# Kernel optimization log

Measured on AMD Instinct MI355X. Metric: run time of the kernel, lower is better.

Reference implementation:

```python
import jax, jax.numpy as jnp
import numpy as np

K = 4            # max_k: top-k proposals kept per gt
IOU_THRESH = 0.6 # Matcher threshold; labels [0,1]


def box_cxcywh_to_xyxy(b):
    cx, cy, w, h = jnp.split(b, 4, axis=-1)
    return jnp.concatenate([cx - 0.5 * w, cy - 0.5 * h, cx + 0.5 * w, cy + 0.5 * h], axis=-1)


def box_iou(b1, b2):
    # b1: [M,4], b2: [N,4] xyxy -> iou [M,N]
    area1 = (b1[:, 2] - b1[:, 0]) * (b1[:, 3] - b1[:, 1])
    area2 = (b2[:, 2] - b2[:, 0]) * (b2[:, 3] - b2[:, 1])
    lt = jnp.maximum(b1[:, None, :2], b2[None, :, :2])
    rb = jnp.minimum(b1[:, None, 2:], b2[None, :, 2:])
    wh = jnp.clip(rb - lt, 0.0)
    inter = wh[..., 0] * wh[..., 1]
    union = area1[:, None] + area2[None, :] - inter
    return inter / jnp.maximum(union, 1e-9)


def setup_inputs() -> dict:
    key = jax.random.key(0)
    k1, k2, k3 = jax.random.split(key, 3)
    B, M, N = 32, 512, 4096
    gt_boxes = jax.random.uniform(k1, (B, M, 4), dtype=jnp.float32)
    proposals = jax.random.uniform(k2, (B, N, 4), dtype=jnp.float32)
    gt_labels = jax.random.randint(k3, (B, M), 0, 80, dtype=jnp.int32)
    return {"gt_boxes": gt_boxes, "proposals": proposals, "gt_labels": gt_labels}


def reference(gt_boxes, proposals, gt_labels):
    # gt_boxes: [B,M,4] cxcywh, proposals: [B,N,4] cxcywh (init_reference)
    B, M, _ = gt_boxes.shape
    N = proposals.shape[1]

    iou = jax.vmap(box_iou)(box_cxcywh_to_xyxy(gt_boxes),
                            box_cxcywh_to_xyxy(proposals))  # [B,M,N]

    # Matcher(thresholds=[0.6], labels=[0,1], allow_low_quality_matches=True)
    matched_idxs = jnp.argmax(iou, axis=1)                 # [B,N] best gt per proposal
    matched_vals = jnp.max(iou, axis=1)                    # [B,N]
    fg = matched_vals >= IOU_THRESH                        # matched_labels == 1
    # low-quality matches: proposals achieving the per-gt max IoU are forced fg
    max_per_gt = jnp.max(iou, axis=2, keepdims=True)       # [B,M,1]
    lq = jnp.any(iou == max_per_gt, axis=1)                # [B,N]
    pos_mask = fg | lq                                     # foreground proposals
    # (labels in [0,80) never equal bg_label=400, matched_labels never -1,
    #  and subsample keeps all fg since num_fg << 0.25*num_queries, so
    #  pos_pr_inds == all foreground proposals.)

    # counts[b,g] = number of fg proposals matched to gt g (unique(return_counts))
    counts = jnp.zeros((B, M), jnp.int32).at[
        jnp.arange(B)[:, None], matched_idxs].add(pos_mask.astype(jnp.int32))

    # sample_topk_per_gt: per-gt top-k by IoU, keep first min(count, k)
    scores, pr_inds = jax.lax.top_k(iou, K)                # [B,M,K]
    valid = jnp.arange(K)[None, None, :] < counts[:, :, None]  # [B,M,K]
    gt_inds = jnp.broadcast_to(jnp.arange(M)[None, :, None], (B, M, K))
    scores = jnp.where(valid, scores, 0.0)
    return scores, pr_inds, gt_inds, valid
```

## Files before the change

### kernel.cpp

```cpp
#include <hip/hip_runtime.h>

#define BB 32
#define MM 512
#define NN 4096
#define KK 4
#define MLO 0.999998f
#define CMG 0.9999995f
#define FG_BITS 0x3F19999A


__device__ __forceinline__ int rfl(int x) {
    return __builtin_amdgcn_readfirstlane(x);
}
__device__ __forceinline__ float rflf(float x) {
    return __int_as_float(rfl(__float_as_int(x)));
}

__device__ __forceinline__ bool beatsI(int v1, int i1, int v2, int i2) {
    return (v1 > v2) || (v1 == v2 && i1 < i2);
}

#define CE(av, ai, bv, bi)                                        \
    {                                                             \
        bool _s = beatsI(bv, bi, av, ai);                         \
        int _mv = _s ? bv : av, _nv = _s ? av : bv;               \
        int _mi = _s ? bi : ai, _ni = _s ? ai : bi;               \
        av = _mv; bv = _nv; ai = _mi; bi = _ni;                   \
    }

struct T4 { int v0, v1, v2, v3; int i0, i1, i2, i3; float thr, c1, thrga; };

__global__ __launch_bounds__(256) void kernA(const float* __restrict__ gt,
                                             const float* __restrict__ pr,
                                             float* __restrict__ topv,
                                             float4* __restrict__ pack,
                                             int* __restrict__ counts,
                                             float* __restrict__ out) {
    const int b = blockIdx.x >> 6;
    const int mblk = blockIdx.x & 63;
    const int tid = threadIdx.x;
    const int wave = rfl(tid >> 6), lane = tid & 63;
    const int mbase = mblk * 8 + wave * 2;
    const float4* g4 = (const float4*)(gt + (size_t)b * MM * 4);
    const float4* p4 = (const float4*)(pr + (size_t)b * NN * 4);

#define GTDEF(G) \
    float gx1_##G, gy1_##G, gx2_##G, gy2_##G, ga_##G; \
    { float4 gg = g4[mbase + G]; \
      float x1 = gg.x - 0.5f * gg.z, y1 = gg.y - 0.5f * gg.w; \
      float x2 = gg.x + 0.5f * gg.z, y2 = gg.y + 0.5f * gg.w; \
      gx1_##G = x1; gy1_##G = y1; gx2_##G = x2; gy2_##G = y2; \
      ga_##G = __fmul_rn(x2 - x1, y2 - y1); }

    GTDEF(0) GTDEF(1)

    T4 t0, t1;

#define PIOU(G, VB) \
    int VB; \
    { float ltx = fmaxf(gx1_##G, px1), lty = fmaxf(gy1_##G, py1); \
      float rbx = fminf(gx2_##G, px2), rby = fminf(gy2_##G, py2); \
      float wc = fmaxf(rbx - ltx, 0.0f), hc = fmaxf(rby - lty, 0.0f); \
      float inter = __fmul_rn(wc, hc); \
      float u = fmaxf((ga_##G + pa) - inter, 1e-9f); \
      VB = __float_as_int(inter / u); }

#define PRIME(T, VB, G) \
    { int x0 = VB, x1 = -1, x2 = -1, x3 = -1; \
      int y0 = lane, y1 = 0x7fffffff, y2 = 0x7fffffff, y3 = 0x7fffffff; \
      for (int off = 1; off < 64; off <<= 1) { \
        int b0 = __shfl_xor(x0, off), b1 = __shfl_xor(x1, off); \
        int b2 = __shfl_xor(x2, off), b3 = __shfl_xor(x3, off); \
        int j0 = __shfl_xor(y0, off), j1 = __shfl_xor(y1, off); \
        int j2 = __shfl_xor(y2, off), j3 = __shfl_xor(y3, off); \
        int z4 = b3, z5 = b2, z6 = b1, z7 = b0; \
        int w4 = j3, w5 = j2, w6 = j1, w7 = j0; \
        CE(x0, y0, z4, w4); CE(x1, y1, z5, w5); \
        CE(x2, y2, z6, w6); CE(x3, y3, z7, w7); \
        CE(x0, y0, x2, y2); CE(x1, y1, x3, y3); \
        CE(x0, y0, x1, y1); CE(x2, y2, x3, y3); \
      } \
      T.v0 = rfl(x0); T.v1 = rfl(x1); T.v2 = rfl(x2); T.v3 = rfl(x3); \
      T.i0 = rfl(y0); T.i1 = rfl(y1); T.i2 = rfl(y2); T.i3 = rfl(y3); \
      T.thr = (T.v3 <= 0) ? 0.0f : rflf(__int_as_float(T.v3) * MLO); \
      T.c1 = 1.0f + T.thr; T.thrga = T.thr * ga_##G; }

    {
        float4 qc = p4[lane];
        float px1 = qc.x - 0.5f * qc.z, py1 = qc.y - 0.5f * qc.w;
        float px2 = qc.x + 0.5f * qc.z, py2 = qc.y + 0.5f * qc.w;
        float pa = __fmul_rn(px2 - px1, py2 - py1);
        PIOU(0, vb0) PIOU(1, vb1)
        PRIME(t0, vb0, 0) PRIME(t1, vb1, 1)
    }

#define COMP(T, G, IN, TR) \
    float IN; bool TR; \
    { float ltx = fmaxf(gx1_##G, px1), lty = fmaxf(gy1_##G, py1); \
      float rbx = fminf(gx2_##G, px2), rby = fminf(gy2_##G, py2); \
      float wc = fmaxf(rbx - ltx, 0.0f), hc = fmaxf(rby - lty, 0.0f); \
      IN = __fmul_rn(wc, hc); \
      TR = IN * T.c1 > __fmaf_rn(T.thr, pa, T.thrga); }

#define MERGE(T, G, MK, IN, TR) \
    if (MK) { \
      float iouv = 0.0f; \
      if (TR) { float uu = fmaxf((ga_##G + pa) - IN, 1e-9f); iouv = IN / uu; } \
      unsigned long long mk = MK; \
      do { \
        int l = __ffsll((unsigned long long)mk) - 1; mk &= mk - 1; \
        int vb = (int)__builtin_amdgcn_readlane(__float_as_int(iouv), l); \
        if (vb > T.v3) {                           \
          int n = nb + l; \
          bool c2 = vb > T.v2, c1c = vb > T.v1, c0 = vb > T.v0; \
          T.v3 = c2 ? T.v2 : vb;                T.i3 = c2 ? T.i2 : n; \
          T.v2 = c2 ? (c1c ? T.v1 : vb) : T.v2; T.i2 = c2 ? (c1c ? T.i1 : n) : T.i2; \
          T.v1 = c1c ? (c0 ? T.v0 : vb) : T.v1; T.i1 = c1c ? (c0 ? T.i0 : n) : T.i1; \
          T.v0 = c0 ? vb : T.v0;                T.i0 = c0 ? n : T.i0; \
        } \
      } while (mk); \
      T.thr = (T.v3 == 0) ? 0.0f : rflf(__int_as_float(T.v3) * MLO); \
      T.c1 = 1.0f + T.thr; T.thrga = T.thr * ga_##G; \
    }

    float4 qn = p4[64 + lane];
    for (int j = 1; j < 64; ++j) {
        float4 qc = qn;
        int jn = (j < 63) ? j + 1 : 63;
        qn = p4[jn * 64 + lane];
        float px1 = qc.x - 0.5f * qc.z, py1 = qc.y - 0.5f * qc.w;
        float px2 = qc.x + 0.5f * qc.z, py2 = qc.y + 0.5f * qc.w;
        float pa = __fmul_rn(px2 - px1, py2 - py1);
        const int nb = j * 64;
        COMP(t0, 0, in0, tr0)
        COMP(t1, 1, in1, tr1)
        unsigned long long mk0 = __ballot(tr0), mk1 = __ballot(tr1);
        if (mk0 | mk1) {
            MERGE(t0, 0, mk0, in0, tr0)
            MERGE(t1, 1, mk1, in1, tr1)
        }
    }

    if (lane == 0) {
        float* pi = out + (size_t)BB * MM * KK;
        float* gi = out + (size_t)2 * BB * MM * KK;
#define WOUT(T, G) \
        { int gm = b * MM + mbase + G; \
          float gmxf = __int_as_float(T.v0); \
          topv[gm * KK + 0] = gmxf; \
          topv[gm * KK + 1] = __int_as_float(T.v1); \
          topv[gm * KK + 2] = __int_as_float(T.v2); \
          topv[gm * KK + 3] = __int_as_float(T.v3); \
          pi[gm * KK + 0] = (float)T.i0; pi[gm * KK + 1] = (float)T.i1; \
          pi[gm * KK + 2] = (float)T.i2; pi[gm * KK + 3] = (float)T.i3; \
          float fm = (float)(mbase + G); \
          gi[gm * KK + 0] = fm; gi[gm * KK + 1] = fm; \
          gi[gm * KK + 2] = fm; gi[gm * KK + 3] = fm; \
          pack[gm * 2 + 0] = make_float4(gx1_##G, gy1_##G, gx2_##G, gy2_##G); \
          pack[gm * 2 + 1] = make_float4(ga_##G, gmxf, gmxf * CMG, 0.0f); \
          counts[gm] = 0; }
        WOUT(t0, 0) WOUT(t1, 1)
    }
}

__global__ __launch_bounds__(256) void kernB(const float* __restrict__ pr,
                                             const float4* __restrict__ pack,
                                             int* __restrict__ counts) {
    __shared__ float4 sG[MM];
    __shared__ float4 sA[MM];
    __shared__ int sV[256], sI[256], sL[256];
    const int b = blockIdx.x >> 6;
    const int nblk = blockIdx.x & 63;
    const int tid = threadIdx.x;

    const float4* gp = pack + (size_t)b * MM * 2;
    for (int i = tid; i < MM; i += 256) {
        sG[i] = gp[i * 2];
        sA[i] = gp[i * 2 + 1];
    }

    const int lane = tid & 63;
    const int qtr = tid >> 6;
    const int m0 = qtr * 128;
    const int n = nblk * 64 + lane;
    float4 qq = ((const float4*)(pr + (size_t)b * NN * 4))[n];
    const float qx1 = qq.x - 0.5f * qq.z, qy1 = qq.y - 0.5f * qq.w;
    const float qx2 = qq.x + 0.5f * qq.z, qy2 = qq.y + 0.5f * qq.w;
    const float pa = __fmul_rn(qx2 - qx1, qy2 - qy1);
    __syncthreads();

    float INb = 0.0f, ub = 1.0f;
    int mb = m0;
    bool closeacc = false;
    int ms = m0, cnt = 0;

    #pragma unroll 4
    for (int mm = 0; mm < 128; ++mm) {
        const int m = m0 + mm;
        float4 gb = sG[m];
        float4 ax = sA[m];
        float ltx = fmaxf(gb.x, qx1), lty = fmaxf(gb.y, qy1);
        float rbx = fminf(gb.z, qx2), rby = fminf(gb.w, qy2);
        float w = fmaxf(rbx - ltx, 0.0f), h = fmaxf(rby - lty, 0.0f);
        float IN = __fmul_rn(w, h);
        float u = fmaxf((ax.x + pa) - IN, 1e-9f);
        float t1 = __fmul_rn(IN, ub);
        float t2 = __fmul_rn(INb, u);
        bool c = t1 > t2;
        closeacc = closeacc || ((t1 > t2 * CMG) && (t2 > t1 * CMG));
        INb = c ? IN : INb;
        ub = c ? u : ub;
        mb = c ? m : mb;
        bool cd = IN >= __fmul_rn(u, ax.z);
        ms = cd ? m : ms;
        cnt += cd ? 1 : 0;
    }

    float bestE;
    {
        float4 gb = sG[mb]; float4 ax = sA[mb];
        float ltx = fmaxf(gb.x, qx1), lty = fmaxf(gb.y, qy1);
        float rbx = fminf(gb.z, qx2), rby = fminf(gb.w, qy2);
        float w = fmaxf(rbx - ltx, 0.0f), h = fmaxf(rby - lty, 0.0f);
        float IN = __fmul_rn(w, h);
        float u = fmaxf((ax.x + pa) - IN, 1e-9f);
        bestE = IN / u;
    }
    bool lqF;
    {
        float4 gb = sG[ms]; float4 ax = sA[ms];
        float ltx = fmaxf(gb.x, qx1), lty = fmaxf(gb.y, qy1);
        float rbx = fminf(gb.z, qx2), rby = fminf(gb.w, qy2);
        float w = fmaxf(rbx - ltx, 0.0f), h = fmaxf(rby - lty, 0.0f);
        float IN = __fmul_rn(w, h);
        float u = fmaxf((ax.x + pa) - IN, 1e-9f);
        lqF = (cnt > 0) && ((IN / u) == ax.y);
    }
    bool need = closeacc || ((cnt >= 2) && !lqF);
    if (__ballot(need) != 0ull) {
        if (need) {
            float bb = 0.0f; int bi = m0; bool ll = false;
            for (int mm = 0; mm < 128; ++mm) {
                const int m = m0 + mm;
                float4 gb = sG[m]; float4 ax = sA[m];
                float ltx = fmaxf(gb.x, qx1), lty = fmaxf(gb.y, qy1);
                float rbx = fminf(gb.z, qx2), rby = fminf(gb.w, qy2);
                float w = fmaxf(rbx - ltx, 0.0f), h = fmaxf(rby - lty, 0.0f);
                float IN = __fmul_rn(w, h);
                float u = fmaxf((ax.x + pa) - IN, 1e-9f);
                float iou = IN / u;
                bool c = iou > bb;
                bb = c ? iou : bb;
                bi = c ? m : bi;
                ll = ll || (iou == ax.y);
            }
            bestE = bb; mb = bi; lqF = ll;
        }
    }

    sV[tid] = __float_as_int(bestE);
    sI[tid] = mb;
    sL[tid] = lqF ? 1 : 0;
    __syncthreads();

    if (tid < 64) {
        int v = sV[tid], i = sI[tid], L = sL[tid];
        #pragma unroll
        for (int q_ = 1; q_ < 4; ++q_) {
            int v2 = sV[tid + q_ * 64], i2 = sI[tid + q_ * 64];
            L |= sL[tid + q_ * 64];
            bool c = v2 > v;
            v = c ? v2 : v;
            i = c ? i2 : i;
        }
        if (v >= FG_BITS || L) {
            atomicAdd(&counts[b * MM + i], 1);
        }
    }
}

__global__ __launch_bounds__(256) void kernC(const float* __restrict__ topv,
                                             const int* __restrict__ counts,
                                             float* __restrict__ out) {
    const int gm = blockIdx.x * 256 + threadIdx.x;
    if (gm >= BB * MM) return;
    const int cnt = counts[gm];
    float* sc = out;
    float* va = out + (size_t)3 * BB * MM * KK;
    #pragma unroll
    for (int k = 0; k < KK; ++k) {
        const bool val = k < cnt;
        sc[gm * KK + k] = val ? topv[gm * KK + k] : 0.0f;
        va[gm * KK + k] = val ? 1.0f : 0.0f;
    }
}

extern "C" void kernel_launch(void* const* d_in, const int* in_sizes, int n_in,
                              void* d_out, int out_size, void* d_ws, size_t ws_size,
                              hipStream_t stream) {
    const float* gt = (const float*)d_in[0];
    const float* pr = (const float*)d_in[1];
    float* out = (float*)d_out;
    char* ws = (char*)d_ws;

    int*    counts = (int*)(ws);
    float*  topv   = (float*)(ws + (1 << 16));
    float4* pack   = (float4*)(ws + (5 << 16));

    kernA<<<BB * (MM / 8), 256, 0, stream>>>(gt, pr, topv, pack, counts, out);
    kernB<<<BB * (NN / 64), 256, 0, stream>>>(pr, pack, counts);
    kernC<<<(BB * MM + 255) / 256, 256, 0, stream>>>(topv, counts, out);
}
```

Measured before the change: 112.2 us.

## Fuse per-gt top-k and per-proposal argmax into one launch, scatter low-quality flags

Kernels A and B become a single launch with two disjoint block ranges, so the per-proposal argmax no longer waits for the per-gt top-k and the two can run concurrently. The per-proposal pass no longer needs the per-gt max, so its low-quality equality check is dropped. Instead a new kernel D scatters low-quality flags from each gt's top-k entries that tie the max, falling back to a full scan over proposals when all four tie. Kernel E then counts matches. This adds two small launches and extra workspace traffic, and the serial full-scan fallback in D could be slow when it is triggered.

```diff
diff --git a/kernel.cpp b/kernel.cpp
--- a/kernel.cpp
+++ b/kernel.cpp
@@ -7,6 +7,7 @@
 #define MLO 0.999998f
 #define CMG 0.9999995f
 #define FG_BITS 0x3F19999A
+#define NA_BLOCKS (BB * (MM / 8))
 
 
 __device__ __forceinline__ int rfl(int x) {
@@ -30,19 +31,28 @@
 
 struct T4 { int v0, v1, v2, v3; int i0, i1, i2, i3; float thr, c1, thrga; };
 
-__global__ __launch_bounds__(256) void kernA(const float* __restrict__ gt,
-                                             const float* __restrict__ pr,
-                                             float* __restrict__ topv,
-                                             float4* __restrict__ pack,
-                                             int* __restrict__ counts,
-                                             float* __restrict__ out) {
-    const int b = blockIdx.x >> 6;
-    const int mblk = blockIdx.x & 63;
-    const int tid = threadIdx.x;
-    const int wave = rfl(tid >> 6), lane = tid & 63;
-    const int mbase = mblk * 8 + wave * 2;
-    const float4* g4 = (const float4*)(gt + (size_t)b * MM * 4);
-    const float4* p4 = (const float4*)(pr + (size_t)b * NN * 4);
+__global__ __launch_bounds__(256) void kernAB(const float* __restrict__ gt,
+                                              const float* __restrict__ pr,
+                                              float* __restrict__ topv,
+                                              int* __restrict__ topi,
+                                              int* __restrict__ counts,
+                                              int* __restrict__ bestv,
+                                              int* __restrict__ bidxA,
+                                              unsigned char* __restrict__ lqflag,
+                                              int* __restrict__ allLq,
+                                              float* __restrict__ out) {
+    __shared__ float4 sG[MM];
+    __shared__ float sAr[MM];
+    __shared__ int sV[256], sI[256];
+
+    if (blockIdx.x < NA_BLOCKS) {
+        const int b = blockIdx.x >> 6;
+        const int mblk = blockIdx.x & 63;
+        const int tid = threadIdx.x;
+        const int wave = rfl(tid >> 6), lane = tid & 63;
+        const int mbase = mblk * 8 + wave * 2;
+        const float4* g4 = (const float4*)(gt + (size_t)b * MM * 4);
+        const float4* p4 = (const float4*)(pr + (size_t)b * NN * 4);
 
 #define GTDEF(G) \
     float gx1_##G, gy1_##G, gx2_##G, gy2_##G, ga_##G; \
@@ -52,9 +62,9 @@
       gx1_##G = x1; gy1_##G = y1; gx2_##G = x2; gy2_##G = y2; \
       ga_##G = __fmul_rn(x2 - x1, y2 - y1); }
 
-    GTDEF(0) GTDEF(1)
-
-    T4 t0, t1;
+        GTDEF(0) GTDEF(1)
+
+        T4 t0, t1;
 
 #define PIOU(G, VB) \
     int VB; \
@@ -85,14 +95,14 @@
       T.thr = (T.v3 <= 0) ? 0.0f : rflf(__int_as_float(T.v3) * MLO); \
       T.c1 = 1.0f + T.thr; T.thrga = T.thr * ga_##G; }
 
-    {
-        float4 qc = p4[lane];
-        float px1 = qc.x - 0.5f * qc.z, py1 = qc.y - 0.5f * qc.w;
-        float px2 = qc.x + 0.5f * qc.z, py2 = qc.y + 0.5f * qc.w;
-        float pa = __fmul_rn(px2 - px1, py2 - py1);
-        PIOU(0, vb0) PIOU(1, vb1)
-        PRIME(t0, vb0, 0) PRIME(t1, vb1, 1)
-    }
+        {
+            float4 qc = p4[lane];
+            float px1 = qc.x - 0.5f * qc.z, py1 = qc.y - 0.5f * qc.w;
+            float px2 = qc.x + 0.5f * qc.z, py2 = qc.y + 0.5f * qc.w;
+            float pa = __fmul_rn(px2 - px1, py2 - py1);
+            PIOU(0, vb0) PIOU(1, vb1)
+            PRIME(t0, vb0, 0) PRIME(t1, vb1, 1)
+        }
 
 #define COMP(T, G, IN, TR) \
     float IN; bool TR; \
@@ -110,7 +120,7 @@
       do { \
         int l = __ffsll((unsigned long long)mk) - 1; mk &= mk - 1; \
         int vb = (int)__builtin_amdgcn_readlane(__float_as_int(iouv), l); \
-        if (vb > T.v3) {                           \
+        if (vb > T.v3) { \
           int n = nb + l; \
           bool c2 = vb > T.v2, c1c = vb > T.v1, c0 = vb > T.v0; \
           T.v3 = c2 ? T.v2 : vb;                T.i3 = c2 ? T.i2 : n; \
@@ -123,160 +133,192 @@
       T.c1 = 1.0f + T.thr; T.thrga = T.thr * ga_##G; \
     }
 
-    float4 qn = p4[64 + lane];
-    for (int j = 1; j < 64; ++j) {
-        float4 qc = qn;
-        int jn = (j < 63) ? j + 1 : 63;
-        qn = p4[jn * 64 + lane];
-        float px1 = qc.x - 0.5f * qc.z, py1 = qc.y - 0.5f * qc.w;
-        float px2 = qc.x + 0.5f * qc.z, py2 = qc.y + 0.5f * qc.w;
-        float pa = __fmul_rn(px2 - px1, py2 - py1);
-        const int nb = j * 64;
-        COMP(t0, 0, in0, tr0)
-        COMP(t1, 1, in1, tr1)
-        unsigned long long mk0 = __ballot(tr0), mk1 = __ballot(tr1);
-        if (mk0 | mk1) {
-            MERGE(t0, 0, mk0, in0, tr0)
-            MERGE(t1, 1, mk1, in1, tr1)
-        }
-    }
-
-    if (lane == 0) {
-        float* pi = out + (size_t)BB * MM * KK;
-        float* gi = out + (size_t)2 * BB * MM * KK;
+        float4 qn = p4[64 + lane];
+        for (int j = 1; j < 64; ++j) {
+            float4 qc = qn;
+            int jn = (j < 63) ? j + 1 : 63;
+            qn = p4[jn * 64 + lane];
+            float px1 = qc.x - 0.5f * qc.z, py1 = qc.y - 0.5f * qc.w;
+            float px2 = qc.x + 0.5f * qc.z, py2 = qc.y + 0.5f * qc.w;
+            float pa = __fmul_rn(px2 - px1, py2 - py1);
+            const int nb = j * 64;
+            COMP(t0, 0, in0, tr0)
+            COMP(t1, 1, in1, tr1)
+            unsigned long long mk0 = __ballot(tr0), mk1 = __ballot(tr1);
+            if (mk0 | mk1) {
+                MERGE(t0, 0, mk0, in0, tr0)
+                MERGE(t1, 1, mk1, in1, tr1)
+            }
+        }
+
+        if (lane == 0) {
+            float* pi = out + (size_t)BB * MM * KK;
+            float* gi = out + (size_t)2 * BB * MM * KK;
 #define WOUT(T, G) \
-        { int gm = b * MM + mbase + G; \
-          float gmxf = __int_as_float(T.v0); \
-          topv[gm * KK + 0] = gmxf; \
-          topv[gm * KK + 1] = __int_as_float(T.v1); \
-          topv[gm * KK + 2] = __int_as_float(T.v2); \
-          topv[gm * KK + 3] = __int_as_float(T.v3); \
-          pi[gm * KK + 0] = (float)T.i0; pi[gm * KK + 1] = (float)T.i1; \
-          pi[gm * KK + 2] = (float)T.i2; pi[gm * KK + 3] = (float)T.i3; \
-          float fm = (float)(mbase + G); \
-          gi[gm * KK + 0] = fm; gi[gm * KK + 1] = fm; \
-          gi[gm * KK + 2] = fm; gi[gm * KK + 3] = fm; \
-          pack[gm * 2 + 0] = make_float4(gx1_##G, gy1_##G, gx2_##G, gy2_##G); \
-          pack[gm * 2 + 1] = make_float4(ga_##G, gmxf, gmxf * CMG, 0.0f); \
-          counts[gm] = 0; }
-        WOUT(t0, 0) WOUT(t1, 1)
-    }
-}
-
-__global__ __launch_bounds__(256) void kernB(const float* __restrict__ pr,
-                                             const float4* __restrict__ pack,
+            { int gm = b * MM + mbase + G; \
+              topv[gm * KK + 0] = __int_as_float(T.v0); \
+              topv[gm * KK + 1] = __int_as_float(T.v1); \
+              topv[gm * KK + 2] = __int_as_float(T.v2); \
+              topv[gm * KK + 3] = __int_as_float(T.v3); \
+              topi[gm * KK + 0] = T.i0; topi[gm * KK + 1] = T.i1; \
+              topi[gm * KK + 2] = T.i2; topi[gm * KK + 3] = T.i3; \
+              pi[gm * KK + 0] = (float)T.i0; pi[gm * KK + 1] = (float)T.i1; \
+              pi[gm * KK + 2] = (float)T.i2; pi[gm * KK + 3] = (float)T.i3; \
+              float fm = (float)(mbase + G); \
+              gi[gm * KK + 0] = fm; gi[gm * KK + 1] = fm; \
+              gi[gm * KK + 2] = fm; gi[gm * KK + 3] = fm; \
+              counts[gm] = 0; }
+            WOUT(t0, 0) WOUT(t1, 1)
+        }
+    } else {
+        const int bid = blockIdx.x - NA_BLOCKS;
+        const int b = bid >> 6;
+        const int nblk = bid & 63;
+        const int tid = threadIdx.x;
+        const float4* g4 = (const float4*)(gt + (size_t)b * MM * 4);
+
+        for (int i = tid; i < MM; i += 256) {
+            float4 gg = g4[i];
+            float x1 = gg.x - 0.5f * gg.z, y1 = gg.y - 0.5f * gg.w;
+            float x2 = gg.x + 0.5f * gg.z, y2 = gg.y + 0.5f * gg.w;
+            sG[i] = make_float4(x1, y1, x2, y2);
+            sAr[i] = __fmul_rn(x2 - x1, y2 - y1);
+        }
+        if (tid < 64) lqflag[(size_t)b * NN + nblk * 64 + tid] = 0;
+        if (tid == 0 && nblk == 0) allLq[b] = 0;
+
+        const int lane = tid & 63;
+        const int qtr = tid >> 6;
+        const int m0 = qtr * 128;
+        const int n = nblk * 64 + lane;
+        float4 qq = ((const float4*)(pr + (size_t)b * NN * 4))[n];
+        const float qx1 = qq.x - 0.5f * qq.z, qy1 = qq.y - 0.5f * qq.w;
+        const float qx2 = qq.x + 0.5f * qq.z, qy2 = qq.y + 0.5f * qq.w;
+        const float pa = __fmul_rn(qx2 - qx1, qy2 - qy1);
+        __syncthreads();
+
+        float INb = 0.0f, ub = 1.0f;
+        int mb = m0;
+        bool closeacc = false;
+
+        #pragma unroll 4
+        for (int mm = 0; mm < 128; ++mm) {
+            const int m = m0 + mm;
+            float4 gb = sG[m];
+            float ar = sAr[m];
+            float ltx = fmaxf(gb.x, qx1), lty = fmaxf(gb.y, qy1);
+            float rbx = fminf(gb.z, qx2), rby = fminf(gb.w, qy2);
+            float w = fmaxf(rbx - ltx, 0.0f), h = fmaxf(rby - lty, 0.0f);
+            float IN = __fmul_rn(w, h);
+            float u = fmaxf((ar + pa) - IN, 1e-9f);
+            float t1 = __fmul_rn(IN, ub);
+            float t2 = __fmul_rn(INb, u);
+            bool c = t1 > t2;
+            closeacc = closeacc || ((t1 > t2 * CMG) && (t2 > t1 * CMG));
+            INb = c ? IN : INb;
+            ub = c ? u : ub;
+            mb = c ? m : mb;
+        }
+
+        float bestE;
+        {
+            float4 gb = sG[mb];
+            float ltx = fmaxf(gb.x, qx1), lty = fmaxf(gb.y, qy1);
+            float rbx = fminf(gb.z, qx2), rby = fminf(gb.w, qy2);
+            float w = fmaxf(rbx - ltx, 0.0f), h = fmaxf(rby - lty, 0.0f);
+            float IN = __fmul_rn(w, h);
+            float u = fmaxf((sAr[mb] + pa) - IN, 1e-9f);
+            bestE = IN / u;
+        }
+        if (__ballot(closeacc) != 0ull) {
+            if (closeacc) {
+                float bb = 0.0f; int bi = m0;
+                for (int mm = 0; mm < 128; ++mm) {
+                    const int m = m0 + mm;
+                    float4 gb = sG[m];
+                    float ltx = fmaxf(gb.x, qx1), lty = fmaxf(gb.y, qy1);
+                    float rbx = fminf(gb.z, qx2), rby = fminf(gb.w, qy2);
+                    float w = fmaxf(rbx - ltx, 0.0f), h = fmaxf(rby - lty, 0.0f);
+                    float IN = __fmul_rn(w, h);
+                    float u = fmaxf((sAr[m] + pa) - IN, 1e-9f);
+                    float iou = IN / u;
+                    bool c = iou > bb;
+                    bb = c ? iou : bb;
+                    bi = c ? m : bi;
+                }
+                bestE = bb; mb = bi;
+            }
+        }
+
+        sV[tid] = __float_as_int(bestE);
+        sI[tid] = mb;
+        __syncthreads();
+
+        if (tid < 64) {
+            int v = sV[tid], i = sI[tid];
+            #pragma unroll
+            for (int q_ = 1; q_ < 4; ++q_) {
+                int v2 = sV[tid + q_ * 64], i2 = sI[tid + q_ * 64];
+                bool c = v2 > v;
+                v = c ? v2 : v;
+                i = c ? i2 : i;
+            }
+            const size_t pidx = (size_t)b * NN + nblk * 64 + tid;
+            bestv[pidx] = v;
+            bidxA[pidx] = i;
+        }
+    }
+}
+
+__global__ __launch_bounds__(256) void kernD(const float* __restrict__ topv,
+                                             const int* __restrict__ topi,
+                                             const float* __restrict__ gt,
+                                             const float* __restrict__ pr,
+                                             unsigned char* __restrict__ lqflag,
+                                             int* __restrict__ allLq) {
+    const int gm = blockIdx.x * 256 + threadIdx.x;
+    if (gm >= BB * MM) return;
+    const int b = gm >> 9, m = gm & (MM - 1);
+    const float v0 = topv[gm * KK + 0];
+    if (v0 == 0.0f) { allLq[b] = 1; return; }
+    unsigned char* fl = lqflag + (size_t)b * NN;
+    fl[topi[gm * KK + 0]] = 1;
+    const float v1 = topv[gm * KK + 1], v2 = topv[gm * KK + 2], v3 = topv[gm * KK + 3];
+    if (v1 == v0) fl[topi[gm * KK + 1]] = 1;
+    if (v2 == v0) fl[topi[gm * KK + 2]] = 1;
+    if (v3 == v0) {
+        fl[topi[gm * KK + 3]] = 1;
+        float4 gg = ((const float4*)(gt + (size_t)b * MM * 4))[m];
+        float x1 = gg.x - 0.5f * gg.z, y1 = gg.y - 0.5f * gg.w;
+        float x2 = gg.x + 0.5f * gg.z, y2 = gg.y + 0.5f * gg.w;
+        float ga = __fmul_rn(x2 - x1, y2 - y1);
+        const float4* p4 = (const float4*)(pr + (size_t)b * NN * 4);
+        for (int n = 0; n < NN; ++n) {
+            float4 qc = p4[n];
+            float px1 = qc.x - 0.5f * qc.z, py1 = qc.y - 0.5f * qc.w;
+            float px2 = qc.x + 0.5f * qc.z, py2 = qc.y + 0.5f * qc.w;
+            float pa = __fmul_rn(px2 - px1, py2 - py1);
+            float ltx = fmaxf(x1, px1), lty = fmaxf(y1, py1);
+            float rbx = fminf(x2, px2), rby = fminf(y2, py2);
+            float w = fmaxf(rbx - ltx, 0.0f), h = fmaxf(rby - lty, 0.0f);
+            float IN = __fmul_rn(w, h);
+            float u = fmaxf((ga + pa) - IN, 1e-9f);
+            if ((IN / u) == v0) fl[n] = 1;
+        }
+    }
+}
+
+__global__ __launch_bounds__(256) void kernE(const int* __restrict__ bestv,
+                                             const int* __restrict__ bidxA,
+                                             const unsigned char* __restrict__ lqflag,
+                                             const int* __restrict__ allLq,
                                              int* __restrict__ counts) {
-    __shared__ float4 sG[MM];
-    __shared__ float4 sA[MM];
-    __shared__ int sV[256], sI[256], sL[256];
-    const int b = blockIdx.x >> 6;
-    const int nblk = blockIdx.x & 63;
-    const int tid = threadIdx.x;
-
-    const float4* gp = pack + (size_t)b * MM * 2;
-    for (int i = tid; i < MM; i += 256) {
-        sG[i] = gp[i * 2];
-        sA[i] = gp[i * 2 + 1];
-    }
-
-    const int lane = tid & 63;
-    const int qtr = tid >> 6;
-    const int m0 = qtr * 128;
-    const int n = nblk * 64 + lane;
-    float4 qq = ((const float4*)(pr + (size_t)b * NN * 4))[n];
-    const float qx1 = qq.x - 0.5f * qq.z, qy1 = qq.y - 0.5f * qq.w;
-    const float qx2 = qq.x + 0.5f * qq.z, qy2 = qq.y + 0.5f * qq.w;
-    const float pa = __fmul_rn(qx2 - qx1, qy2 - qy1);
-    __syncthreads();
-
-    float INb = 0.0f, ub = 1.0f;
-    int mb = m0;
-    bool closeacc = false;
-    int ms = m0, cnt = 0;
-
-    #pragma unroll 4
-    for (int mm = 0; mm < 128; ++mm) {
-        const int m = m0 + mm;
-        float4 gb = sG[m];
-        float4 ax = sA[m];
-        float ltx = fmaxf(gb.x, qx1), lty = fmaxf(gb.y, qy1);
-        float rbx = fminf(gb.z, qx2), rby = fminf(gb.w, qy2);
-        float w = fmaxf(rbx - ltx, 0.0f), h = fmaxf(rby - lty, 0.0f);
-        float IN = __fmul_rn(w, h);
-        float u = fmaxf((ax.x + pa) - IN, 1e-9f);
-        float t1 = __fmul_rn(IN, ub);
-        float t2 = __fmul_rn(INb, u);
-        bool c = t1 > t2;
-        closeacc = closeacc || ((t1 > t2 * CMG) && (t2 > t1 * CMG));
-        INb = c ? IN : INb;
-        ub = c ? u : ub;
-        mb = c ? m : mb;
-        bool cd = IN >= __fmul_rn(u, ax.z);
-        ms = cd ? m : ms;
-        cnt += cd ? 1 : 0;
-    }
-
-    float bestE;
-    {
-        float4 gb = sG[mb]; float4 ax = sA[mb];
-        float ltx = fmaxf(gb.x, qx1), lty = fmaxf(gb.y, qy1);
-        float rbx = fminf(gb.z, qx2), rby = fminf(gb.w, qy2);
-        float w = fmaxf(rbx - ltx, 0.0f), h = fmaxf(rby - lty, 0.0f);
-        float IN = __fmul_rn(w, h);
-        float u = fmaxf((ax.x + pa) - IN, 1e-9f);
-        bestE = IN / u;
-    }
-    bool lqF;
-    {
-        float4 gb = sG[ms]; float4 ax = sA[ms];
-        float ltx = fmaxf(gb.x, qx1), lty = fmaxf(gb.y, qy1);
-        float rbx = fminf(gb.z, qx2), rby = fminf(gb.w, qy2);
-        float w = fmaxf(rbx - ltx, 0.0f), h = fmaxf(rby - lty, 0.0f);
-        float IN = __fmul_rn(w, h);
-        float u = fmaxf((ax.x + pa) - IN, 1e-9f);
-        lqF = (cnt > 0) && ((IN / u) == ax.y);
-    }
-    bool need = closeacc || ((cnt >= 2) && !lqF);
-    if (__ballot(need) != 0ull) {
-        if (need) {
-            float bb = 0.0f; int bi = m0; bool ll = false;
-            for (int mm = 0; mm < 128; ++mm) {
-                const int m = m0 + mm;
-                float4 gb = sG[m]; float4 ax = sA[m];
-                float ltx = fmaxf(gb.x, qx1), lty = fmaxf(gb.y, qy1);
-                float rbx = fminf(gb.z, qx2), rby = fminf(gb.w, qy2);
-                float w = fmaxf(rbx - ltx, 0.0f), h = fmaxf(rby - lty, 0.0f);
-                float IN = __fmul_rn(w, h);
-                float u = fmaxf((ax.x + pa) - IN, 1e-9f);
-                float iou = IN / u;
-                bool c = iou > bb;
-                bb = c ? iou : bb;
-                bi = c ? m : bi;
-                ll = ll || (iou == ax.y);
-            }
-            bestE = bb; mb = bi; lqF = ll;
-        }
-    }
-
-    sV[tid] = __float_as_int(bestE);
-    sI[tid] = mb;
-    sL[tid] = lqF ? 1 : 0;
-    __syncthreads();
-
-    if (tid < 64) {
-        int v = sV[tid], i = sI[tid], L = sL[tid];
-        #pragma unroll
-        for (int q_ = 1; q_ < 4; ++q_) {
-            int v2 = sV[tid + q_ * 64], i2 = sI[tid + q_ * 64];
-            L |= sL[tid + q_ * 64];
-            bool c = v2 > v;
-            v = c ? v2 : v;
-            i = c ? i2 : i;
-        }
-        if (v >= FG_BITS || L) {
-            atomicAdd(&counts[b * MM + i], 1);
-        }
-    }
+    const int idx = blockIdx.x * 256 + threadIdx.x;
+    const int b = idx >> 12;
+    const int bb = bestv[idx];
+    const int mi = bidxA[idx];
+    const bool pos = (bb >= FG_BITS) || lqflag[idx] || (allLq[b] != 0);
+    if (pos) atomicAdd(&counts[b * MM + mi], 1);
 }
 
 __global__ __launch_bounds__(256) void kernC(const float* __restrict__ topv,
@@ -303,11 +345,17 @@
     float* out = (float*)d_out;
     char* ws = (char*)d_ws;
 
-    int*    counts = (int*)(ws);
-    float*  topv   = (float*)(ws + (1 << 16));
-    float4* pack   = (float4*)(ws + (5 << 16));
-
-    kernA<<<BB * (MM / 8), 256, 0, stream>>>(gt, pr, topv, pack, counts, out);
-    kernB<<<BB * (NN / 64), 256, 0, stream>>>(pr, pack, counts);
+    int*           counts = (int*)(ws);
+    float*         topv   = (float*)(ws + (1 << 16));
+    int*           topi   = (int*)(ws + (5 << 16));
+    int*           bestv  = (int*)(ws + (9 << 16));
+    int*           bidxA  = (int*)(ws + (17 << 16));
+    unsigned char* lqflag = (unsigned char*)(ws + (25 << 16));
+    int*           allLq  = (int*)(ws + (27 << 16));
+
+    kernAB<<<2 * NA_BLOCKS, 256, 0, stream>>>(gt, pr, topv, topi, counts,
+                                              bestv, bidxA, lqflag, allLq, out);
+    kernD<<<(BB * MM + 255) / 256, 256, 0, stream>>>(topv, topi, gt, pr, lqflag, allLq);
+    kernE<<<(BB * NN) / 256, 256, 0, stream>>>(bestv, bidxA, lqflag, allLq, counts);
     kernC<<<(BB * MM + 255) / 256, 256, 0, stream>>>(topv, counts, out);
 }
```

Result: faster. 94.76 us (-15.5%).
